# Kernel optimization log

Hardware: AMD Instinct MI355X
Metric: run time of the kernel (lower is better)

Reference implementation:

```python
import jax, jax.numpy as jnp
import numpy as np

D, E, FF = 512, 8, 4 * 512
BS, H, W = 2, 32, 32
T = BS * H * W


def setup_inputs() -> dict:
    key = jax.random.key(0)
    ks = jax.random.split(key, 12)
    s = lambda fan_in: 1.0 / np.sqrt(fan_in)
    return {
        "x": jax.random.normal(ks[0], (BS, D, H, W), dtype=jnp.float32),
        "Wg": jax.random.normal(ks[1], (D, E), dtype=jnp.float32) * s(D),
        "bg": jnp.zeros((E,), dtype=jnp.float32),
        "Wn": jax.random.normal(ks[2], (D, E), dtype=jnp.float32) * s(D),
        "bn": jnp.zeros((E,), dtype=jnp.float32),
        "W1": jax.random.normal(ks[3], (E, D, FF), dtype=jnp.float32) * s(D),
        "b1": jnp.zeros((E, FF), dtype=jnp.float32),
        "W2": jax.random.normal(ks[4], (E, FF, D), dtype=jnp.float32) * s(FF),
        "b2": jnp.zeros((E, D), dtype=jnp.float32),
        "noise_eps": jax.random.normal(ks[5], (T, E), dtype=jnp.float32),
        "top_k": 2,
    }


def reference(x, Wg, bg, Wn, bn, W1, b1, W2, b2, noise_eps, top_k):
    bs, d, h, w = x.shape
    tokens = x.transpose(0, 2, 3, 1).reshape(-1, d)  # [T, d]
    t = tokens.shape[0]
    # Noisy top-k router
    logits = tokens @ Wg + bg                                  # [T, E]
    noise = noise_eps * jax.nn.softplus(tokens @ Wn + bn)      # [T, E]
    noisy = logits + noise
    top_v, top_i = jax.lax.top_k(noisy, top_k)                 # [T, k]
    sparse = jnp.full_like(noisy, -jnp.inf)
    sparse = sparse.at[jnp.arange(t)[:, None], top_i].set(top_v)
    gates = jax.nn.softmax(sparse, axis=-1)                    # [T, E], zero off top-k
    # Expert MLPs (dense over experts; gates zero-out non-selected)
    hdn = jax.nn.relu(jnp.einsum("td,edf->tef", tokens, W1) + b1)  # [T, E, 4d]
    out_e = jnp.einsum("tef,efd->ted", hdn, W2) + b2               # [T, E, d]
    out = jnp.einsum("te,ted->td", gates, out_e)                   # combine
    return out.reshape(bs, h, w, d).transpose(0, 3, 1, 2)
```

## Files before the change

kernel.cpp:

```cpp
#include <hip/hip_runtime.h>
#include <hip/hip_bf16.h>
#include <math.h>

#define DD  512
#define EE  8
#define FFD 2048
#define TT  2048
#define HWH 1024

typedef __bf16 b16x8 __attribute__((ext_vector_type(8)));
typedef float  f32x4 __attribute__((ext_vector_type(4)));

__device__ __forceinline__ unsigned short f2bf(float f) {
    unsigned u = __builtin_bit_cast(unsigned, f);
    u = (u + 0x7FFFu + ((u >> 16) & 1u)) >> 16;
    return (unsigned short)u;
}

__device__ __forceinline__ void gload16(const void* g, void* l) {
    __builtin_amdgcn_global_load_lds(
        (const __attribute__((address_space(1))) void*)g,
        (__attribute__((address_space(3))) void*)l, 16, 0, 0);
}

__device__ __forceinline__ int seg_pred(const int* __restrict__ cnt, int e) {
    int s = 0;
    #pragma unroll
    for (int i = 0; i < EE; ++i) s += (i < e) ? cnt[i] : 0;
    return s;
}

__global__ __launch_bounds__(256) void moe_prep(
    const float* __restrict__ W1, const float* __restrict__ W2,
    const float* __restrict__ x,
    unsigned short* __restrict__ W1t, unsigned short* __restrict__ W2t,
    unsigned short* __restrict__ xb,
    const float* __restrict__ Wg, const float* __restrict__ Wn,
    float* __restrict__ part)
{
    __shared__ float ld[64][65];
    int which = blockIdx.z, e = blockIdx.y;

    if (which == 3) {
        if (blockIdx.x >= 32) return;
        int u = threadIdx.x & 63;
        int q = threadIdx.x >> 6;
        int tt = blockIdx.x, dc = e;
        int t = tt * 64 + u;
        int b = t >> 10, hw = t & 1023;
        const float* xp = x + (size_t)b * DD * HWH + hw;
        int d0 = dc * 64 + q * 16;
        float accL[EE], accN[EE];
        #pragma unroll
        for (int k = 0; k < EE; ++k) { accL[k] = 0.f; accN[k] = 0.f; }
        #pragma unroll
        for (int i = 0; i < 16; ++i) {
            int d = d0 + i;
            float tv = xp[(size_t)d * HWH];
            #pragma unroll
            for (int k = 0; k < EE; ++k) {
                accL[k] = fmaf(tv, Wg[d * EE + k], accL[k]);
                accN[k] = fmaf(tv, Wn[d * EE + k], accN[k]);
            }
        }
        float (*s)[64][16] = (float (*)[64][16])&ld[0][0];
        #pragma unroll
        for (int k = 0; k < EE; ++k) { s[q][u][k] = accL[k]; s[q][u][k + 8] = accN[k]; }
        __syncthreads();
        int idx = threadIdx.x * 4;
        int ot = idx >> 4, oc = idx & 15;
        float4 v;
        v.x = s[0][ot][oc+0] + s[1][ot][oc+0] + s[2][ot][oc+0] + s[3][ot][oc+0];
        v.y = s[0][ot][oc+1] + s[1][ot][oc+1] + s[2][ot][oc+1] + s[3][ot][oc+1];
        v.z = s[0][ot][oc+2] + s[1][ot][oc+2] + s[2][ot][oc+2] + s[3][ot][oc+2];
        v.w = s[0][ot][oc+3] + s[1][ot][oc+3] + s[2][ot][oc+3] + s[3][ot][oc+3];
        *(float4*)&part[((size_t)dc * TT + tt * 64 + ot) * 16 + oc] = v;
        return;
    }

    const float* in; unsigned short* out; int R, C;
    if (which == 0)      { R = DD;  C = FFD; in = W1 + (size_t)e*DD*FFD; out = W1t + (size_t)e*FFD*DD; }
    else if (which == 1) { R = FFD; C = DD;  in = W2 + (size_t)e*FFD*DD; out = W2t + (size_t)e*DD*FFD; }
    else { if (e >= 2) return; R = DD; C = HWH; in = x + (size_t)e*DD*HWH; out = xb + (size_t)e*HWH*DD; }
    int tilesC = C >> 6;
    if ((int)blockIdx.x >= (R >> 6) * tilesC) return;
    int tr = (blockIdx.x / tilesC) << 6, tc = (blockIdx.x % tilesC) << 6;
    int ty = threadIdx.x >> 4, tx = threadIdx.x & 15;
    #pragma unroll
    for (int i = 0; i < 4; ++i) {
        const float4 v = *(const float4*)&in[(size_t)(tr + ty + i*16)*C + tc + tx*4];
        ld[ty + i*16][tx*4+0] = v.x; ld[ty + i*16][tx*4+1] = v.y;
        ld[ty + i*16][tx*4+2] = v.z; ld[ty + i*16][tx*4+3] = v.w;
    }
    __syncthreads();
    #pragma unroll
    for (int i = 0; i < 4; ++i) {
        int c = ty + i*16;
        unsigned o0 = f2bf(ld[tx*4+0][c]) | ((unsigned)f2bf(ld[tx*4+1][c]) << 16);
        unsigned o1 = f2bf(ld[tx*4+2][c]) | ((unsigned)f2bf(ld[tx*4+3][c]) << 16);
        *(uint2*)&out[(size_t)(tc + c)*R + tr + tx*4] = make_uint2(o0, o1);
    }
}

__global__ __launch_bounds__(256) void moe_router_topk(
    const float* __restrict__ part,
    const float* __restrict__ bg, const float* __restrict__ bn,
    const float* __restrict__ neps,
    int* __restrict__ cnt, int* __restrict__ pair0, int* __restrict__ pair1,
    int* __restrict__ ltok, float* __restrict__ lgate)
{
    int t = blockIdx.x * 256 + threadIdx.x;
    float L[EE], N[EE];
    #pragma unroll
    for (int e = 0; e < EE; ++e) { L[e] = bg[e]; N[e] = bn[e]; }
    #pragma unroll
    for (int dc = 0; dc < 8; ++dc) {
        const float* p = &part[((size_t)dc * TT + t) * 16];
        float4 a0 = *(const float4*)&p[0];
        float4 a1 = *(const float4*)&p[4];
        float4 a2 = *(const float4*)&p[8];
        float4 a3 = *(const float4*)&p[12];
        L[0] += a0.x; L[1] += a0.y; L[2] += a0.z; L[3] += a0.w;
        L[4] += a1.x; L[5] += a1.y; L[6] += a1.z; L[7] += a1.w;
        N[0] += a2.x; N[1] += a2.y; N[2] += a2.z; N[3] += a2.w;
        N[4] += a3.x; N[5] += a3.y; N[6] += a3.z; N[7] += a3.w;
    }
    float noisy[EE];
    #pragma unroll
    for (int e = 0; e < EE; ++e) {
        float sp = fmaxf(N[e], 0.f) + log1pf(expf(-fabsf(N[e])));
        noisy[e] = L[e] + neps[t * EE + e] * sp;
    }
    int e0 = 0; float v0 = noisy[0];
    #pragma unroll
    for (int e = 1; e < EE; ++e) if (noisy[e] > v0) { v0 = noisy[e]; e0 = e; }
    int e1 = (e0 == 0) ? 1 : 0; float v1 = noisy[e1];
    #pragma unroll
    for (int e = 0; e < EE; ++e)
        if (e != e0 && e != e1 && noisy[e] > v1) { v1 = noisy[e]; e1 = e; }
    float ex  = expf(v1 - v0);
    float inv = 1.f / (1.f + ex);
    float g0 = inv, g1 = ex * inv;
    int p0 = atomicAdd(&cnt[e0], 1);
    int p1 = atomicAdd(&cnt[e1], 1);
    ltok[e0 * TT + p0] = t; lgate[e0 * TT + p0] = g0;
    ltok[e1 * TT + p1] = t; lgate[e1 * TT + p1] = g1;
    pair0[t] = (e0 << 16) | p0;
    pair1[t] = (e1 << 16) | p1;
}

__global__ __launch_bounds__(256, 3) void moe_gemm1(
    const unsigned short* __restrict__ xb, const unsigned short* __restrict__ W1t,
    const float* __restrict__ b1, const int* __restrict__ cnt,
    const int* __restrict__ ltok, unsigned short* __restrict__ Hbuf)
{
    int e = blockIdx.x, mt = blockIdx.y, nt = blockIdx.z;
    int ce = cnt[e];
    if (mt * 64 >= ce) return;
    int s0 = seg_pred(cnt, e);
    const unsigned short* Be = W1t + (size_t)e * FFD * DD;
    __shared__ unsigned short As[2][64 * 64];
    __shared__ unsigned short Bs[2][128 * 64];
    int tid = threadIdx.x, lane = tid & 63, wv = tid >> 6;

    int srow = lane >> 3, schunk = lane & 7;
    int srcoff = ((schunk ^ srow) << 3);

    size_t aoff[2]; int ards[2];
    #pragma unroll
    for (int c = 0; c < 2; ++c) {
        int r0 = (c*4 + wv)*8;
        int ri = mt*64 + r0 + srow;
        int tok = ltok[e * TT + (ri < ce ? ri : 0)];
        aoff[c] = (size_t)tok * DD + srcoff;
        ards[c] = r0 * 64;
    }
    size_t boff[4]; int brds[4];
    #pragma unroll
    for (int c = 0; c < 4; ++c) {
        int r0 = (c*4 + wv)*8;
        boff[c] = (size_t)(nt*128 + r0 + srow) * DD + srcoff;
        brds[c] = r0 * 64;
    }

    int frow = lane & 15, fk = (lane >> 4) * 8;
    int am = (wv >> 1) * 32, bnn = (wv & 1) * 64;
    int rx = (frow & 7) << 3;

    f32x4 acc[2][4];
    f32x4 zero = {0.f, 0.f, 0.f, 0.f};
    #pragma unroll
    for (int m = 0; m < 2; ++m)
        #pragma unroll
        for (int n = 0; n < 4; ++n) acc[m][n] = zero;

    #pragma unroll
    for (int c = 0; c < 2; ++c) gload16(&xb[aoff[c]], &As[0][ards[c]]);
    #pragma unroll
    for (int c = 0; c < 4; ++c) gload16(&Be[boff[c]], &Bs[0][brds[c]]);
    #pragma unroll
    for (int c = 0; c < 2; ++c) gload16(&xb[aoff[c] + 64], &As[1][ards[c]]);
    #pragma unroll
    for (int c = 0; c < 4; ++c) gload16(&Be[boff[c] + 64], &Bs[1][brds[c]]);

    #pragma unroll
    for (int t = 0; t < 8; ++t) {
        if (t < 6) { asm volatile("s_waitcnt vmcnt(6)" ::: "memory"); }
        else       { asm volatile("s_waitcnt vmcnt(0)" ::: "memory"); }
        __builtin_amdgcn_s_barrier();
        __builtin_amdgcn_sched_barrier(0);
        const int cur = t & 1;
        #pragma unroll
        for (int k2 = 0; k2 < 64; k2 += 32) {
            b16x8 af[2], bf[4];
            #pragma unroll
            for (int m = 0; m < 2; ++m)
                af[m] = *(const b16x8*)&As[cur][(am + m*16 + frow)*64 + ((k2 + fk) ^ rx)];
            #pragma unroll
            for (int n = 0; n < 4; ++n)
                bf[n] = *(const b16x8*)&Bs[cur][(bnn + n*16 + frow)*64 + ((k2 + fk) ^ rx)];
            #pragma unroll
            for (int m = 0; m < 2; ++m)
                #pragma unroll
                for (int n = 0; n < 4; ++n)
                    acc[m][n] = __builtin_amdgcn_mfma_f32_16x16x32_bf16(af[m], bf[n], acc[m][n], 0, 0, 0);
        }
        __builtin_amdgcn_s_barrier();
        if (t < 6) {
            int kk = (t + 2) * 64;
            #pragma unroll
            for (int c = 0; c < 2; ++c) gload16(&xb[aoff[c] + kk], &As[cur][ards[c]]);
            #pragma unroll
            for (int c = 0; c < 4; ++c) gload16(&Be[boff[c] + kk], &Bs[cur][brds[c]]);
        }
    }

    int crow = (lane >> 4) * 4;
    #pragma unroll
    for (int m = 0; m < 2; ++m) {
        #pragma unroll
        for (int i = 0; i < 4; ++i) {
            int r = mt*64 + am + m*16 + crow + i;
            if (r < ce) {
                size_t hrow = (size_t)(s0 + r) * FFD;
                #pragma unroll
                for (int n = 0; n < 4; ++n) {
                    int col = nt*128 + bnn + n*16 + frow;
                    float v = acc[m][n][i] + b1[e * FFD + col];
                    Hbuf[hrow + col] = f2bf(fmaxf(v, 0.f));
                }
            }
        }
    }
}

__global__ __launch_bounds__(256, 3) void moe_gemm2(
    const unsigned short* __restrict__ Hbuf, const unsigned short* __restrict__ W2t,
    const int* __restrict__ cnt, float* __restrict__ P4)
{
    int e = blockIdx.x, mt = blockIdx.y;
    int split = blockIdx.z >> 2, nt = blockIdx.z & 3;
    int ce = cnt[e];
    if (mt * 64 >= ce) return;
    int s0 = seg_pred(cnt, e);
    int kbase = split * 512;
    const unsigned short* Be = W2t + (size_t)e * DD * FFD;
    __shared__ unsigned short As[2][64 * 64];
    __shared__ unsigned short Bs[2][128 * 64];
    int tid = threadIdx.x, lane = tid & 63, wv = tid >> 6;

    int srow = lane >> 3, schunk = lane & 7;
    int srcoff = ((schunk ^ srow) << 3);

    size_t aoff[2]; int ards[2];
    #pragma unroll
    for (int c = 0; c < 2; ++c) {
        int r0 = (c*4 + wv)*8;
        int g = s0 + mt*64 + r0 + srow; if (g > 4095) g = 4095;
        aoff[c] = (size_t)g * FFD + kbase + srcoff;
        ards[c] = r0 * 64;
    }
    size_t boff[4]; int brds[4];
    #pragma unroll
    for (int c = 0; c < 4; ++c) {
        int r0 = (c*4 + wv)*8;
        boff[c] = (size_t)(nt*128 + r0 + srow) * FFD + kbase + srcoff;
        brds[c] = r0 * 64;
    }

    int frow = lane & 15, fk = (lane >> 4) * 8;
    int am = (wv >> 1) * 32, bnn = (wv & 1) * 64;
    int rx = (frow & 7) << 3;

    f32x4 acc[2][4];
    f32x4 zero = {0.f, 0.f, 0.f, 0.f};
    #pragma unroll
    for (int m = 0; m < 2; ++m)
        #pragma unroll
        for (int n = 0; n < 4; ++n) acc[m][n] = zero;

    #pragma unroll
    for (int c = 0; c < 2; ++c) gload16(&Hbuf[aoff[c]], &As[0][ards[c]]);
    #pragma unroll
    for (int c = 0; c < 4; ++c) gload16(&Be[boff[c]], &Bs[0][brds[c]]);
    #pragma unroll
    for (int c = 0; c < 2; ++c) gload16(&Hbuf[aoff[c] + 64], &As[1][ards[c]]);
    #pragma unroll
    for (int c = 0; c < 4; ++c) gload16(&Be[boff[c] + 64], &Bs[1][brds[c]]);

    #pragma unroll
    for (int t = 0; t < 8; ++t) {
        if (t < 6) { asm volatile("s_waitcnt vmcnt(6)" ::: "memory"); }
        else       { asm volatile("s_waitcnt vmcnt(0)" ::: "memory"); }
        __builtin_amdgcn_s_barrier();
        __builtin_amdgcn_sched_barrier(0);
        const int cur = t & 1;
        #pragma unroll
        for (int k2 = 0; k2 < 64; k2 += 32) {
            b16x8 af[2], bf[4];
            #pragma unroll
            for (int m = 0; m < 2; ++m)
                af[m] = *(const b16x8*)&As[cur][(am + m*16 + frow)*64 + ((k2 + fk) ^ rx)];
            #pragma unroll
            for (int n = 0; n < 4; ++n)
                bf[n] = *(const b16x8*)&Bs[cur][(bnn + n*16 + frow)*64 + ((k2 + fk) ^ rx)];
            #pragma unroll
            for (int m = 0; m < 2; ++m)
                #pragma unroll
                for (int n = 0; n < 4; ++n)
                    acc[m][n] = __builtin_amdgcn_mfma_f32_16x16x32_bf16(af[m], bf[n], acc[m][n], 0, 0, 0);
        }
        __builtin_amdgcn_s_barrier();
        if (t < 6) {
            int kk = (t + 2) * 64;
            #pragma unroll
            for (int c = 0; c < 2; ++c) gload16(&Hbuf[aoff[c] + kk], &As[cur][ards[c]]);
            #pragma unroll
            for (int c = 0; c < 4; ++c) gload16(&Be[boff[c] + kk], &Bs[cur][brds[c]]);
        }
    }

    int crow = (lane >> 4) * 4;
    float* Pw = P4 + (size_t)split * 4096 * DD;
    #pragma unroll
    for (int m = 0; m < 2; ++m) {
        #pragma unroll
        for (int i = 0; i < 4; ++i) {
            int r = mt*64 + am + m*16 + crow + i;
            if (r < ce) {
                size_t prow = (size_t)(s0 + r) * DD;
                #pragma unroll
                for (int n = 0; n < 4; ++n) {
                    int col = nt*128 + bnn + n*16 + frow;
                    Pw[prow + col] = acc[m][n][i];
                }
            }
        }
    }
}

__global__ __launch_bounds__(256) void moe_combine(
    const int* __restrict__ pair0, const int* __restrict__ pair1,
    const int* __restrict__ cnt, const float* __restrict__ lgate,
    const float* __restrict__ b2, const float* __restrict__ P4,
    float* __restrict__ out)
{
    __shared__ float tile[32][68];
    int tid = threadIdx.x;
    int ti = blockIdx.x, dc = blockIdx.y;
    int ty = tid >> 3, tx = tid & 7;
    int t = ti * 32 + ty;
    int a0 = pair0[t], a1 = pair1[t];
    int e0 = a0 >> 16, sl0 = a0 & 0xFFFF;
    int e1 = a1 >> 16, sl1 = a1 & 0xFFFF;
    int p0 = seg_pred(cnt, e0) + sl0, p1 = seg_pred(cnt, e1) + sl1;
    float g0 = lgate[e0 * TT + sl0], g1 = lgate[e1 * TT + sl1];
    int d0 = dc * 64 + tx * 8;
    f32x4 s0v[2] = {{0,0,0,0},{0,0,0,0}}, s1v[2] = {{0,0,0,0},{0,0,0,0}};
    #pragma unroll
    for (int s = 0; s < 4; ++s) {
        const f32x4* r0p = (const f32x4*)(P4 + ((size_t)s * 4096 + p0) * DD + d0);
        const f32x4* r1p = (const f32x4*)(P4 + ((size_t)s * 4096 + p1) * DD + d0);
        s0v[0] += r0p[0]; s0v[1] += r0p[1];
        s1v[0] += r1p[0]; s1v[1] += r1p[1];
    }
    const f32x4* b0p = (const f32x4*)(b2 + e0 * DD + d0);
    const f32x4* b1p = (const f32x4*)(b2 + e1 * DD + d0);
    #pragma unroll
    for (int q = 0; q < 2; ++q) {
        f32x4 v = g0 * (s0v[q] + b0p[q]) + g1 * (s1v[q] + b1p[q]);
        *(f32x4*)&tile[ty][tx*8 + q*4] = v;
    }
    __syncthreads();
    int dy = tid >> 2, hx = tid & 3;
    int b = (ti * 32) >> 10, hw0 = (ti * 32) & 1023;
    size_t obase = ((size_t)(b * DD + dc * 64 + dy)) * HWH + hw0;
    #pragma unroll
    for (int q = 0; q < 2; ++q) {
        int j = hx * 8 + q * 4;
        float4 w;
        w.x = tile[j + 0][dy];
        w.y = tile[j + 1][dy];
        w.z = tile[j + 2][dy];
        w.w = tile[j + 3][dy];
        *(float4*)&out[obase + j] = w;
    }
}

extern "C" void kernel_launch(void* const* d_in, const int* in_sizes, int n_in,
                              void* d_out, int out_size, void* d_ws, size_t ws_size,
                              hipStream_t stream)
{
    const float* x    = (const float*)d_in[0];
    const float* Wg   = (const float*)d_in[1];
    const float* bg   = (const float*)d_in[2];
    const float* Wn   = (const float*)d_in[3];
    const float* bn   = (const float*)d_in[4];
    const float* W1   = (const float*)d_in[5];
    const float* b1   = (const float*)d_in[6];
    const float* W2   = (const float*)d_in[7];
    const float* b2   = (const float*)d_in[8];
    const float* neps = (const float*)d_in[9];

    char* ws = (char*)d_ws;
    int*   cnt   = (int*)(ws + 0);
    int*   pair0 = (int*)(ws + 512);
    int*   pair1 = (int*)(ws + 8704);
    int*   ltok  = (int*)(ws + 32768);
    float* lgate = (float*)(ws + 98304);
    float* part  = (float*)(ws + 163840);
    unsigned short* xb   = (unsigned short*)(ws + 1212416);
    unsigned short* Hbuf = (unsigned short*)(ws + 3309568);
    unsigned short* W1t  = (unsigned short*)(ws + 20086784);
    unsigned short* W2t  = (unsigned short*)(ws + 36864000);
    float*          P4   = (float*)(ws + 53641216);

    hipMemsetAsync(cnt, 0, 32, stream);
    moe_prep<<<dim3(256, 8, 4), 256, 0, stream>>>(W1, W2, x, W1t, W2t, xb, Wg, Wn, part);
    moe_router_topk<<<TT / 256, 256, 0, stream>>>(part, bg, bn, neps,
                                                  cnt, pair0, pair1, ltok, lgate);
    moe_gemm1<<<dim3(EE, 32, 16), 256, 0, stream>>>(xb, W1t, b1, cnt, ltok, Hbuf);
    moe_gemm2<<<dim3(EE, 32, 16), 256, 0, stream>>>(Hbuf, W2t, cnt, P4);
    moe_combine<<<dim3(TT / 32, 8), 256, 0, stream>>>(pair0, pair1, cnt, lgate, b2, P4, (float*)d_out);
}
```

Baseline: 102.0 us.

## Fold count reset into prep, widen transpose tiles, halve gemm2 split-K

Removes the separate memset by zeroing the expert counters inside the prep kernel. The prep transpose now handles 128x64 tiles per block and writes 16-byte bf16 stores, using half as many blocks. gemm2 goes from split-K=4 to split-K=2 with twice as many K iterations per block, so combine reads two partials instead of four. The trade-off is fewer gemm2 blocks (less parallelism and latency hiding) in exchange for less partial-sum traffic and one fewer launch.

```diff
diff --git a/kernel.cpp b/kernel.cpp
--- a/kernel.cpp
+++ b/kernel.cpp
@@ -36,15 +36,17 @@
     unsigned short* __restrict__ W1t, unsigned short* __restrict__ W2t,
     unsigned short* __restrict__ xb,
     const float* __restrict__ Wg, const float* __restrict__ Wn,
-    float* __restrict__ part)
-{
-    __shared__ float ld[64][65];
+    float* __restrict__ part, int* __restrict__ cnt)
+{
+    __shared__ float ld[128][65];
     int which = blockIdx.z, e = blockIdx.y;
+    int tid = threadIdx.x;
 
     if (which == 3) {
+        if (e == 0 && blockIdx.x == 0 && tid < EE) cnt[tid] = 0;
         if (blockIdx.x >= 32) return;
-        int u = threadIdx.x & 63;
-        int q = threadIdx.x >> 6;
+        int u = tid & 63;
+        int q = tid >> 6;
         int tt = blockIdx.x, dc = e;
         int t = tt * 64 + u;
         int b = t >> 10, hw = t & 1023;
@@ -67,7 +69,7 @@
         #pragma unroll
         for (int k = 0; k < EE; ++k) { s[q][u][k] = accL[k]; s[q][u][k + 8] = accN[k]; }
         __syncthreads();
-        int idx = threadIdx.x * 4;
+        int idx = tid * 4;
         int ot = idx >> 4, oc = idx & 15;
         float4 v;
         v.x = s[0][ot][oc+0] + s[1][ot][oc+0] + s[2][ot][oc+0] + s[3][ot][oc+0];
@@ -82,23 +84,28 @@
     if (which == 0)      { R = DD;  C = FFD; in = W1 + (size_t)e*DD*FFD; out = W1t + (size_t)e*FFD*DD; }
     else if (which == 1) { R = FFD; C = DD;  in = W2 + (size_t)e*FFD*DD; out = W2t + (size_t)e*DD*FFD; }
     else { if (e >= 2) return; R = DD; C = HWH; in = x + (size_t)e*DD*HWH; out = xb + (size_t)e*HWH*DD; }
-    int tilesC = C >> 6;
-    if ((int)blockIdx.x >= (R >> 6) * tilesC) return;
-    int tr = (blockIdx.x / tilesC) << 6, tc = (blockIdx.x % tilesC) << 6;
-    int ty = threadIdx.x >> 4, tx = threadIdx.x & 15;
-    #pragma unroll
-    for (int i = 0; i < 4; ++i) {
-        const float4 v = *(const float4*)&in[(size_t)(tr + ty + i*16)*C + tc + tx*4];
-        ld[ty + i*16][tx*4+0] = v.x; ld[ty + i*16][tx*4+1] = v.y;
-        ld[ty + i*16][tx*4+2] = v.z; ld[ty + i*16][tx*4+3] = v.w;
+    int tilesC = C >> 6, tilesR = R >> 7;
+    if ((int)blockIdx.x >= tilesR * tilesC) return;
+    int tr = (blockIdx.x / tilesC) << 7, tc = (blockIdx.x % tilesC) << 6;
+    int ty = tid >> 4, tx = tid & 15;
+    #pragma unroll
+    for (int i = 0; i < 8; ++i) {
+        int r = ty + i * 16;
+        const float4 v = *(const float4*)&in[(size_t)(tr + r)*C + tc + tx*4];
+        ld[r][tx*4+0] = v.x; ld[r][tx*4+1] = v.y;
+        ld[r][tx*4+2] = v.z; ld[r][tx*4+3] = v.w;
     }
     __syncthreads();
-    #pragma unroll
-    for (int i = 0; i < 4; ++i) {
-        int c = ty + i*16;
-        unsigned o0 = f2bf(ld[tx*4+0][c]) | ((unsigned)f2bf(ld[tx*4+1][c]) << 16);
-        unsigned o1 = f2bf(ld[tx*4+2][c]) | ((unsigned)f2bf(ld[tx*4+3][c]) << 16);
-        *(uint2*)&out[(size_t)(tc + c)*R + tr + tx*4] = make_uint2(o0, o1);
+    int ox = tid & 15;
+    #pragma unroll
+    for (int it = 0; it < 4; ++it) {
+        int c = (tid >> 4) + it * 16;
+        uint4 u;
+        u.x = f2bf(ld[ox*8+0][c]) | ((unsigned)f2bf(ld[ox*8+1][c]) << 16);
+        u.y = f2bf(ld[ox*8+2][c]) | ((unsigned)f2bf(ld[ox*8+3][c]) << 16);
+        u.z = f2bf(ld[ox*8+4][c]) | ((unsigned)f2bf(ld[ox*8+5][c]) << 16);
+        u.w = f2bf(ld[ox*8+6][c]) | ((unsigned)f2bf(ld[ox*8+7][c]) << 16);
+        *(uint4*)&out[(size_t)(tc + c)*R + tr + ox*8] = u;
     }
 }
 
@@ -256,14 +263,14 @@
 
 __global__ __launch_bounds__(256, 3) void moe_gemm2(
     const unsigned short* __restrict__ Hbuf, const unsigned short* __restrict__ W2t,
-    const int* __restrict__ cnt, float* __restrict__ P4)
+    const int* __restrict__ cnt, float* __restrict__ P2)
 {
     int e = blockIdx.x, mt = blockIdx.y;
     int split = blockIdx.z >> 2, nt = blockIdx.z & 3;
     int ce = cnt[e];
     if (mt * 64 >= ce) return;
     int s0 = seg_pred(cnt, e);
-    int kbase = split * 512;
+    int kbase = split * 1024;
     const unsigned short* Be = W2t + (size_t)e * DD * FFD;
     __shared__ unsigned short As[2][64 * 64];
     __shared__ unsigned short Bs[2][128 * 64];
@@ -309,9 +316,9 @@
     for (int c = 0; c < 4; ++c) gload16(&Be[boff[c] + 64], &Bs[1][brds[c]]);
 
     #pragma unroll
-    for (int t = 0; t < 8; ++t) {
-        if (t < 6) { asm volatile("s_waitcnt vmcnt(6)" ::: "memory"); }
-        else       { asm volatile("s_waitcnt vmcnt(0)" ::: "memory"); }
+    for (int t = 0; t < 16; ++t) {
+        if (t < 14) { asm volatile("s_waitcnt vmcnt(6)" ::: "memory"); }
+        else        { asm volatile("s_waitcnt vmcnt(0)" ::: "memory"); }
         __builtin_amdgcn_s_barrier();
         __builtin_amdgcn_sched_barrier(0);
         const int cur = t & 1;
@@ -331,7 +338,7 @@
                     acc[m][n] = __builtin_amdgcn_mfma_f32_16x16x32_bf16(af[m], bf[n], acc[m][n], 0, 0, 0);
         }
         __builtin_amdgcn_s_barrier();
-        if (t < 6) {
+        if (t < 14) {
             int kk = (t + 2) * 64;
             #pragma unroll
             for (int c = 0; c < 2; ++c) gload16(&Hbuf[aoff[c] + kk], &As[cur][ards[c]]);
@@ -341,7 +348,7 @@
     }
 
     int crow = (lane >> 4) * 4;
-    float* Pw = P4 + (size_t)split * 4096 * DD;
+    float* Pw = P2 + (size_t)split * 4096 * DD;
     #pragma unroll
     for (int m = 0; m < 2; ++m) {
         #pragma unroll
@@ -362,7 +369,7 @@
 __global__ __launch_bounds__(256) void moe_combine(
     const int* __restrict__ pair0, const int* __restrict__ pair1,
     const int* __restrict__ cnt, const float* __restrict__ lgate,
-    const float* __restrict__ b2, const float* __restrict__ P4,
+    const float* __restrict__ b2, const float* __restrict__ P2,
     float* __restrict__ out)
 {
     __shared__ float tile[32][68];
@@ -378,9 +385,9 @@
     int d0 = dc * 64 + tx * 8;
     f32x4 s0v[2] = {{0,0,0,0},{0,0,0,0}}, s1v[2] = {{0,0,0,0},{0,0,0,0}};
     #pragma unroll
-    for (int s = 0; s < 4; ++s) {
-        const f32x4* r0p = (const f32x4*)(P4 + ((size_t)s * 4096 + p0) * DD + d0);
-        const f32x4* r1p = (const f32x4*)(P4 + ((size_t)s * 4096 + p1) * DD + d0);
+    for (int s = 0; s < 2; ++s) {
+        const f32x4* r0p = (const f32x4*)(P2 + ((size_t)s * 4096 + p0) * DD + d0);
+        const f32x4* r1p = (const f32x4*)(P2 + ((size_t)s * 4096 + p1) * DD + d0);
         s0v[0] += r0p[0]; s0v[1] += r0p[1];
         s1v[0] += r1p[0]; s1v[1] += r1p[1];
     }
@@ -433,13 +440,12 @@
     unsigned short* Hbuf = (unsigned short*)(ws + 3309568);
     unsigned short* W1t  = (unsigned short*)(ws + 20086784);
     unsigned short* W2t  = (unsigned short*)(ws + 36864000);
-    float*          P4   = (float*)(ws + 53641216);
-
-    hipMemsetAsync(cnt, 0, 32, stream);
-    moe_prep<<<dim3(256, 8, 4), 256, 0, stream>>>(W1, W2, x, W1t, W2t, xb, Wg, Wn, part);
+    float*          P2   = (float*)(ws + 53641216);
+
+    moe_prep<<<dim3(128, 8, 4), 256, 0, stream>>>(W1, W2, x, W1t, W2t, xb, Wg, Wn, part, cnt);
     moe_router_topk<<<TT / 256, 256, 0, stream>>>(part, bg, bn, neps,
                                                   cnt, pair0, pair1, ltok, lgate);
     moe_gemm1<<<dim3(EE, 32, 16), 256, 0, stream>>>(xb, W1t, b1, cnt, ltok, Hbuf);
-    moe_gemm2<<<dim3(EE, 32, 16), 256, 0, stream>>>(Hbuf, W2t, cnt, P4);
-    moe_combine<<<dim3(TT / 32, 8), 256, 0, stream>>>(pair0, pair1, cnt, lgate, b2, P4, (float*)d_out);
-}
+    moe_gemm2<<<dim3(EE, 32, 8), 256, 0, stream>>>(Hbuf, W2t, cnt, P2);
+    moe_combine<<<dim3(TT / 32, 8), 256, 0, stream>>>(pair0, pair1, cnt, lgate, b2, P2, (float*)d_out);
+}
```

Result: faster. 91.42 us (-10.4%).
